# Optimization experiments

Hardware: AMD Instinct MI355X
Metric: run time of the kernel (lower is better)

The kernel has to match this reference:

```python
import jax, jax.numpy as jnp
import numpy as np

B, D, H = 256, 512, 256
K = 5
MARGIN = 1.0
TAU = 1.0
LAM_C = 0.01
LAM_E = 0.1
BETA = 0.1
LN_EPS = 1e-5


def _layernorm(x, g, b):
    mu = jnp.mean(x, axis=-1, keepdims=True)
    var = jnp.var(x, axis=-1, keepdims=True)
    return (x - mu) * jax.lax.rsqrt(var + LN_EPS) * g + b


def setup_inputs() -> dict:
    key = jax.random.key(0)
    ks = jax.random.split(key, 16)
    s = 0.02
    inp = {
        "outputs": jax.random.normal(ks[0], (B, 3, 64, 64), jnp.float32),
        "images": jax.random.normal(ks[1], (B, 3, 64, 64), jnp.float32),
        "f_orig": jax.random.normal(ks[2], (B, D), jnp.float32),
        "f_recon": jax.random.normal(ks[3], (B, D), jnp.float32),
        "cf1": jax.random.normal(ks[4], (B, 256, 8, 8), jnp.float32),
        "cf2": jax.random.normal(ks[5], (B, 512, 4, 4), jnp.float32),
        # EnergyNet encoder params
        "W1": jax.random.normal(ks[6], (D, H), jnp.float32) * s,
        "b1": jnp.zeros((H,), jnp.float32),
        "g1": jnp.ones((H,), jnp.float32),
        "be1": jnp.zeros((H,), jnp.float32),
        "W2": jax.random.normal(ks[7], (H, H), jnp.float32) * s,
        "b2": jnp.zeros((H,), jnp.float32),
        # EnergyNet interaction params
        "W3": jax.random.normal(ks[8], (3 * H, H), jnp.float32) * s,
        "b3": jnp.zeros((H,), jnp.float32),
        "g3": jnp.ones((H,), jnp.float32),
        "be3": jnp.zeros((H,), jnp.float32),
        "W4": jax.random.normal(ks[9], (H, H // 2), jnp.float32) * s,
        "b4": jnp.zeros((H // 2,), jnp.float32),
        "W5": jax.random.normal(ks[10], (H // 2, 1), jnp.float32) * s,
        "b5": jnp.zeros((1,), jnp.float32),
    }
    return inp


def _encoder(x, W1, b1, g1, be1, W2, b2):
    h = _layernorm(x @ W1 + b1, g1, be1)
    return jax.nn.relu(h) @ W2 + b2


def _energy_matrix(f1, f2, W1, b1, g1, be1, W2, b2, W3, b3, g3, be3, W4, b4, W5, b5):
    e1 = _encoder(f1, W1, b1, g1, be1, W2, b2)  # [B,H]
    e2 = _encoder(f2, W1, b1, g1, be1, W2, b2)  # [B,H]
    e1b = jnp.broadcast_to(e1[:, None, :], (B, B, H))
    e2b = jnp.broadcast_to(e2[None, :, :], (B, B, H))
    combined = jnp.concatenate([e1b, e2b, e1b * e2b], axis=-1)  # [B,B,3H]
    h = jax.nn.relu(_layernorm(combined @ W3 + b3, g3, be3))
    h = jax.nn.relu(h @ W4 + b4)
    return (h @ W5 + b5)[..., 0]  # [B,B]


def _topk_neighbors(f, k):
    fn = f / (jnp.linalg.norm(f, axis=1, keepdims=True))
    sim = fn @ fn.T
    sim = jnp.where(jnp.eye(f.shape[0], dtype=bool), -jnp.inf, sim)
    _, idx = jax.lax.top_k(sim, k)  # [B,k]
    onehot = jnp.zeros((f.shape[0], f.shape[0]), jnp.float32)
    rows = jnp.arange(f.shape[0])[:, None]
    return onehot.at[rows, idx].set(1.0)


def _entropy(x):
    xn = (x - x.min()) / (x.max() - x.min() + 1e-8)
    # torch.histc(bins=256, min=0, max=1): values at max go to last bin
    idx = jnp.clip(jnp.floor(xn.reshape(-1) * 256.0).astype(jnp.int32), 0, 255)
    hist = jnp.bincount(idx, length=256).astype(jnp.float32)
    p = hist / hist.sum()
    return -jnp.sum(p * jnp.log2(p + 1e-8))


def reference(outputs, images, f_orig, f_recon, cf1, cf2,
              W1, b1, g1, be1, W2, b2, W3, b3, g3, be3, W4, b4, W5, b5):
    # reconstruction loss
    recon = jnp.mean((outputs - images) ** 2)

    # energy margin loss
    E = _energy_matrix(f_orig, f_recon, W1, b1, g1, be1, W2, b2,
                       W3, b3, g3, be3, W4, b4, W5, b5)
    pos = jnp.diag(E)[:, None]
    losses = jax.nn.relu(MARGIN + E - pos)
    neg_mask = ~jnp.eye(B, dtype=bool)
    standard_loss = jnp.sum(losses * neg_mask) / (B * (B - 1))

    k = min(K, B - 1)
    on = _topk_neighbors(f_orig, k)
    rn = _topk_neighbors(f_recon, k)
    inter = jnp.sum(on * rn, axis=1)
    union = jnp.sum(jnp.clip(on + rn, 0.0, 1.0), axis=1)
    jaccard = inter / (union + 1e-8)
    neighbor_loss = 1.0 - jnp.mean(jaccard)
    energy_loss = standard_loss + 0.3 * neighbor_loss

    # compression loss over the dict of compressed features {cf1, cf2}
    sp = 0.5 * (jnp.mean(jnp.abs(cf1)) + jnp.mean(jnp.abs(cf2)))
    en = 0.5 * (_entropy(cf1) + _entropy(cf2))
    compress = sp + BETA * en

    total = recon + LAM_C * compress + LAM_E * energy_loss
    return (total, recon, energy_loss, compress)
```

## Files before the change

kernel.cpp:

```cpp
#include <hip/hip_runtime.h>
#include <math.h>

typedef __attribute__((ext_vector_type(8))) short short8;
typedef __attribute__((ext_vector_type(4))) float f32x4;


__device__ __forceinline__ float wave_sum(float v) {
#pragma unroll
    for (int o = 32; o > 0; o >>= 1) v += __shfl_down(v, o);
    return v;
}

__device__ __forceinline__ float block_sum256(float v, float* red) {
    v = wave_sum(v);
    int t = threadIdx.x;
    if ((t & 63) == 0) red[t >> 6] = v;
    __syncthreads();
    float r = red[0] + red[1] + red[2] + red[3];
    __syncthreads();
    return r;
}

__device__ __forceinline__ unsigned fenc(float f) {
    unsigned u = __float_as_uint(f);
    return (u & 0x80000000u) ? ~u : (u | 0x80000000u);
}
__device__ __forceinline__ float fdec(unsigned u) {
    return (u & 0x80000000u) ? __uint_as_float(u & 0x7fffffffu) : __uint_as_float(~u);
}

__device__ __forceinline__ ushort f2bf(float f) {
    unsigned u = __float_as_uint(f);
    unsigned r = (u + 0x7fffu + ((u >> 16) & 1u)) >> 16;
    return (ushort)r;
}


__global__ void init_kernel(float* wsf, unsigned* wsu, int* wsi) {
    int t = threadIdx.x;
    if (t < 7) wsf[t] = 0.f;
    if (t == 7 || t == 9) wsu[t] = 0xFFFFFFFFu;
    if (t == 8 || t == 10) wsu[t] = 0u;
    wsi[16 + t] = 0;
    wsi[272 + t] = 0;
}

__global__ void recon_kernel(const float4* __restrict__ o, const float4* __restrict__ im,
                             int n4, float* acc) {
    __shared__ float red[4];
    float s = 0.f;
    for (int i = blockIdx.x * blockDim.x + threadIdx.x; i < n4; i += gridDim.x * blockDim.x) {
        float4 a = o[i], b = im[i];
        float dx = a.x - b.x, dy = a.y - b.y, dz = a.z - b.z, dw = a.w - b.w;
        s += dx * dx + dy * dy + dz * dz + dw * dw;
    }
    float tot = block_sum256(s, red);
    if (threadIdx.x == 0) atomicAdd(acc, tot);
}

__global__ void absmm_kernel(const float4* __restrict__ x, int n4,
                             float* absAcc, unsigned* mnAcc, unsigned* mxAcc) {
    __shared__ float red[4];
    __shared__ float rmn[4], rmx[4];
    float s = 0.f, mn = INFINITY, mx = -INFINITY;
    for (int i = blockIdx.x * blockDim.x + threadIdx.x; i < n4; i += gridDim.x * blockDim.x) {
        float4 a = x[i];
        s += fabsf(a.x) + fabsf(a.y) + fabsf(a.z) + fabsf(a.w);
        mn = fminf(mn, fminf(fminf(a.x, a.y), fminf(a.z, a.w)));
        mx = fmaxf(mx, fmaxf(fmaxf(a.x, a.y), fmaxf(a.z, a.w)));
    }
    float tot = block_sum256(s, red);
#pragma unroll
    for (int o = 32; o > 0; o >>= 1) {
        mn = fminf(mn, __shfl_down(mn, o));
        mx = fmaxf(mx, __shfl_down(mx, o));
    }
    int t = threadIdx.x;
    if ((t & 63) == 0) { rmn[t >> 6] = mn; rmx[t >> 6] = mx; }
    __syncthreads();
    if (t == 0) {
        atomicAdd(absAcc, tot);
        float m1 = fminf(fminf(rmn[0], rmn[1]), fminf(rmn[2], rmn[3]));
        float m2 = fmaxf(fmaxf(rmx[0], rmx[1]), fmaxf(rmx[2], rmx[3]));
        atomicMin(mnAcc, fenc(m1));
        atomicMax(mxAcc, fenc(m2));
    }
}

__global__ void hist_kernel(const float4* __restrict__ x, int n4,
                            const unsigned* mm, int* hist) {
    __shared__ int hl[256];
    hl[threadIdx.x] = 0;
    __syncthreads();
    float mn = fdec(mm[0]), mx = fdec(mm[1]);
    float inv = 256.f / (mx - mn + 1e-8f);
    for (int i = blockIdx.x * blockDim.x + threadIdx.x; i < n4; i += gridDim.x * blockDim.x) {
        float4 a = x[i];
        int b0 = min(max((int)floorf((a.x - mn) * inv), 0), 255);
        int b1 = min(max((int)floorf((a.y - mn) * inv), 0), 255);
        int b2 = min(max((int)floorf((a.z - mn) * inv), 0), 255);
        int b3 = min(max((int)floorf((a.w - mn) * inv), 0), 255);
        atomicAdd(&hl[b0], 1);
        atomicAdd(&hl[b1], 1);
        atomicAdd(&hl[b2], 1);
        atomicAdd(&hl[b3], 1);
    }
    __syncthreads();
    if (hl[threadIdx.x]) atomicAdd(&hist[threadIdx.x], hl[threadIdx.x]);
}

__global__ void entropy_kernel(const int* h1, const int* h2, float* out, float n1, float n2) {
    __shared__ float red[4];
    int t = threadIdx.x;
    float p1 = (float)h1[t] / n1;
    float p2 = (float)h2[t] / n2;
    float e1 = -p1 * log2f(p1 + 1e-8f);
    float e2 = -p2 * log2f(p2 + 1e-8f);
    float s1 = block_sum256(e1, red);
    float s2 = block_sum256(e2, red);
    if (t == 0) { out[0] = s1; out[1] = s2; }
}

__global__ void norm_kernel(const float4* __restrict__ fo, const float4* __restrict__ fr,
                            float* rnorm) {
    __shared__ float red[4];
    int r = blockIdx.x;
    const float4* f = (r < 256) ? (fo + (size_t)r * 128) : (fr + (size_t)(r - 256) * 128);
    float s = 0.f;
    if (threadIdx.x < 128) {
        float4 a = f[threadIdx.x];
        s = a.x * a.x + a.y * a.y + a.z * a.z + a.w * a.w;
    }
    float tot = block_sum256(s, red);
    if (threadIdx.x == 0) rnorm[r] = 1.0f / sqrtf(tot);
}

__global__ void encoder_kernel(const float* __restrict__ f_orig, const float* __restrict__ f_recon,
                               const float* __restrict__ W1, const float* __restrict__ b1,
                               const float* __restrict__ g1, const float* __restrict__ be1,
                               const float* __restrict__ W2, const float* __restrict__ b2,
                               const float* __restrict__ W3,
                               float* __restrict__ eAll, float* __restrict__ Aall) {
    int r = blockIdx.x;
    int t = threadIdx.x;
    const float* f = (r < 256) ? (f_orig + (size_t)r * 512) : (f_recon + (size_t)(r - 256) * 512);
    const float* W3p = (r < 256) ? W3 : (W3 + 256 * 256);
    __shared__ float fs[512];
    __shared__ float hs[256];
    __shared__ float es[256];
    __shared__ float red[4];
    fs[t] = f[t];
    fs[t + 256] = f[t + 256];
    __syncthreads();
    float x = b1[t];
    for (int k = 0; k < 512; ++k) x += fs[k] * W1[k * 256 + t];
    float s1 = block_sum256(x, red);
    float s2 = block_sum256(x * x, red);
    float mean = s1 * (1.f / 256.f);
    float var = s2 * (1.f / 256.f) - mean * mean;
    float rstd = rsqrtf(var + 1e-5f);
    float hn = (x - mean) * rstd * g1[t] + be1[t];
    hs[t] = fmaxf(hn, 0.f);
    __syncthreads();
    float e = b2[t];
    for (int k = 0; k < 256; ++k) e += hs[k] * W2[k * 256 + t];
    eAll[(size_t)r * 256 + t] = e;
    es[t] = e;
    __syncthreads();
    float a = 0.f;
    for (int k = 0; k < 256; ++k) a += es[k] * W3p[k * 256 + t];
    Aall[(size_t)r * 256 + t] = a;
}

__global__ void topk_kernel(const float4* __restrict__ fo, const float4* __restrict__ fr,
                            const float* __restrict__ rnorm, float* jacAcc) {
    int i = blockIdx.x, t = threadIdx.x;
    __shared__ float4 fis[128];
    __shared__ float sv[256];
    __shared__ int si[256];
    __shared__ int O[5], R[5];
    for (int pass = 0; pass < 2; ++pass) {
        const float4* f = pass ? fr : fo;
        const float* rn = pass ? (rnorm + 256) : rnorm;
        if (t < 128) fis[t] = f[(size_t)i * 128 + t];
        __syncthreads();
        float dot = 0.f;
        const float4* frow = f + (size_t)t * 128;
        for (int k = 0; k < 128; ++k) {
            float4 a = fis[k], b = frow[k];
            dot += a.x * b.x + a.y * b.y + a.z * b.z + a.w * b.w;
        }
        float simv = dot * rn[i] * rn[t];
        if (t == i) simv = -INFINITY;
        int chosen = 0;
        for (int r5 = 0; r5 < 5; ++r5) {
            sv[t] = chosen ? -INFINITY : simv;
            si[t] = t;
            __syncthreads();
            for (int s = 128; s > 0; s >>= 1) {
                if (t < s) {
                    if (sv[t + s] > sv[t] || (sv[t + s] == sv[t] && si[t + s] < si[t])) {
                        sv[t] = sv[t + s];
                        si[t] = si[t + s];
                    }
                }
                __syncthreads();
            }
            int wIdx = si[0];
            if (t == wIdx) chosen = 1;
            if (t == 0) { if (pass) R[r5] = wIdx; else O[r5] = wIdx; }
            __syncthreads();
        }
        __syncthreads();
    }
    if (t == 0) {
        int inter = 0;
#pragma unroll
        for (int a = 0; a < 5; ++a)
#pragma unroll
            for (int b = 0; b < 5; ++b) inter += (O[a] == R[b]);
        float fi2 = (float)inter;
        float jac = fi2 / (10.f - fi2 + 1e-8f);
        atomicAdd(jacAcc, jac);
    }
}

__global__ void pack_w3_kernel(const float* __restrict__ W3c, ushort* __restrict__ W3p) {
    int s = blockIdx.x * 256 + threadIdx.x;
    int lane = s & 63;
    int tt = (s >> 6) & 15;
    int kk = s >> 10;
    int qq = lane >> 4, nn = lane & 15;
    int tcol = tt * 16 + nn;
    short8 v;
#pragma unroll
    for (int jj = 0; jj < 8; ++jj) {
        int k = kk * 32 + qq * 8 + jj;
        v[jj] = (short)f2bf(W3c[(size_t)k * 256 + tcol]);
    }
    *(short8*)(W3p + (size_t)s * 8) = v;
}

__global__ void pack_w4_kernel(const float* __restrict__ W4, ushort* __restrict__ W4p) {
    int s = blockIdx.x * 256 + threadIdx.x;
    int lane = s & 63;
    int tt = (s >> 6) & 7;
    int kk = s >> 9;
    int qq = lane >> 4, nn = lane & 15;
    int ncol = tt * 16 + nn;
    short8 v;
#pragma unroll
    for (int jj = 0; jj < 8; ++jj) {
        int k = kk * 32 + qq * 8 + jj;
        v[jj] = (short)f2bf(W4[(size_t)k * 128 + ncol]);
    }
    *(short8*)(W4p + (size_t)s * 8) = v;
}

__global__ __launch_bounds__(256) void energy_mfma_kernel(
    const float* __restrict__ eAll, const float* __restrict__ Aall,
    const ushort* __restrict__ W3p, const ushort* __restrict__ W4p,
    const float* __restrict__ b3, const float* __restrict__ g3, const float* __restrict__ be3,
    const float* __restrict__ b4, const float* __restrict__ W5, const float* __restrict__ b5,
    float* __restrict__ E)
{
    int i = blockIdx.x >> 2;
    int jq = blockIdx.x & 3;
    int t = threadIdx.x;
    int w = t >> 6;
    int lane = t & 63;
    int q = lane >> 4;
    int n = lane & 15;
    int jbase = jq * 64 + w * 16;

    __shared__ float comb[256], g3s[256], be3s[256];
    __shared__ uint4 Bst[1024];
    __shared__ __align__(16) ushort Hs[4][16 * 264];

    const float* e1 = eAll + (size_t)i * 256;
    const float* e2 = eAll + 65536;
    const float* A1 = Aall + (size_t)i * 256;
    const float* A2 = Aall + 65536;

    comb[t] = A1[t] + b3[t];
    g3s[t] = g3[t];
    be3s[t] = be3[t];

    f32x4 acc[16];
#pragma unroll
    for (int x = 0; x < 16; ++x) acc[x] = (f32x4){0.f, 0.f, 0.f, 0.f};

    const float* e2row = e2 + (size_t)(jbase + n) * 256;

    for (int kk = 0; kk < 8; ++kk) {
        __syncthreads();
        {
            const uint4* src = (const uint4*)(W3p + (size_t)kk * 8192);
#pragma unroll
            for (int x = 0; x < 4; ++x) Bst[t * 4 + x] = src[t * 4 + x];
        }
        int kb = kk * 32 + q * 8;
        float4 ea0 = *(const float4*)(e2row + kb);
        float4 ea1 = *(const float4*)(e2row + kb + 4);
        float4 eb0 = *(const float4*)(e1 + kb);
        float4 eb1 = *(const float4*)(e1 + kb + 4);
        short8 af;
        af[0] = (short)f2bf(ea0.x * eb0.x);
        af[1] = (short)f2bf(ea0.y * eb0.y);
        af[2] = (short)f2bf(ea0.z * eb0.z);
        af[3] = (short)f2bf(ea0.w * eb0.w);
        af[4] = (short)f2bf(ea1.x * eb1.x);
        af[5] = (short)f2bf(ea1.y * eb1.y);
        af[6] = (short)f2bf(ea1.z * eb1.z);
        af[7] = (short)f2bf(ea1.w * eb1.w);
        __syncthreads();
        const short8* bst = (const short8*)Bst;
#pragma unroll
        for (int tt = 0; tt < 16; ++tt) {
            short8 bfr = bst[tt * 64 + lane];
            acc[tt] = __builtin_amdgcn_mfma_f32_16x16x32_bf16(af, bfr, acc[tt], 0, 0, 0);
        }
    }

    float s1[4] = {0.f, 0.f, 0.f, 0.f}, s2[4] = {0.f, 0.f, 0.f, 0.f};
#pragma unroll
    for (int tt = 0; tt < 16; ++tt) {
        int col = tt * 16 + n;
        float cb = comb[col];
#pragma unroll
        for (int r = 0; r < 4; ++r) {
            int jr = jbase + q * 4 + r;
            float v = acc[tt][r] + cb + A2[(size_t)jr * 256 + col];
            acc[tt][r] = v;
            s1[r] += v;
            s2[r] += v * v;
        }
    }
#pragma unroll
    for (int off = 1; off < 16; off <<= 1) {
#pragma unroll
        for (int r = 0; r < 4; ++r) {
            s1[r] += __shfl_xor(s1[r], off);
            s2[r] += __shfl_xor(s2[r], off);
        }
    }
    float mean[4], rstd[4];
#pragma unroll
    for (int r = 0; r < 4; ++r) {
        mean[r] = s1[r] * (1.f / 256.f);
        float var = s2[r] * (1.f / 256.f) - mean[r] * mean[r];
        rstd[r] = rsqrtf(var + 1e-5f);
    }
    ushort* hrow = Hs[w];
#pragma unroll
    for (int tt = 0; tt < 16; ++tt) {
        int col = tt * 16 + n;
        float gg = g3s[col], be = be3s[col];
#pragma unroll
        for (int r = 0; r < 4; ++r) {
            float hv = fmaxf((acc[tt][r] - mean[r]) * rstd[r] * gg + be, 0.f);
            hrow[(q * 4 + r) * 264 + col] = f2bf(hv);
        }
    }

    f32x4 gacc[8];
#pragma unroll
    for (int x = 0; x < 8; ++x) gacc[x] = (f32x4){0.f, 0.f, 0.f, 0.f};

    for (int kk = 0; kk < 8; ++kk) {
        __syncthreads();
        {
            const uint4* src = (const uint4*)(W4p + (size_t)kk * 4096);
#pragma unroll
            for (int x = 0; x < 2; ++x) Bst[t * 2 + x] = src[t * 2 + x];
        }
        short8 af = *(const short8*)(hrow + n * 264 + kk * 32 + q * 8);
        __syncthreads();
        const short8* bst = (const short8*)Bst;
#pragma unroll
        for (int tt = 0; tt < 8; ++tt) {
            short8 bfr = bst[tt * 64 + lane];
            gacc[tt] = __builtin_amdgcn_mfma_f32_16x16x32_bf16(af, bfr, gacc[tt], 0, 0, 0);
        }
    }

    float ep[4] = {0.f, 0.f, 0.f, 0.f};
    float b5v = b5[0];
#pragma unroll
    for (int tt = 0; tt < 8; ++tt) {
        int col = tt * 16 + n;
        float b4v = b4[col], w5v = W5[col];
#pragma unroll
        for (int r = 0; r < 4; ++r)
            ep[r] += fmaxf(gacc[tt][r] + b4v, 0.f) * w5v;
    }
#pragma unroll
    for (int off = 1; off < 16; off <<= 1) {
#pragma unroll
        for (int r = 0; r < 4; ++r) ep[r] += __shfl_xor(ep[r], off);
    }
    if (n == 0) {
#pragma unroll
        for (int r = 0; r < 4; ++r)
            E[(size_t)i * 256 + jbase + q * 4 + r] = ep[r] + b5v;
    }
}

__global__ void margin_kernel(const float* __restrict__ E, float* slAcc) {
    __shared__ float red[4];
    int i = blockIdx.x, t = threadIdx.x;
    float diag = E[(size_t)i * 256 + i];
    float l = (t == i) ? 0.f : fmaxf(1.f + E[(size_t)i * 256 + t] - diag, 0.f);
    float tot = block_sum256(l, red);
    if (t == 0) atomicAdd(slAcc, tot);
}

__global__ void finalize_kernel(const float* wsf, float* out) {
    if (threadIdx.x == 0 && blockIdx.x == 0) {
        float recon = wsf[0] / 3145728.f;
        float sp = 0.5f * (wsf[1] / 4194304.f + wsf[2] / 2097152.f);
        float en = 0.5f * (wsf[3] + wsf[4]);
        float compress = sp + 0.1f * en;
        float sl = wsf[5] / (256.f * 255.f);
        float nl = 1.f - wsf[6] / 256.f;
        float energy = sl + 0.3f * nl;
        float total = recon + 0.01f * compress + 0.1f * energy;
        out[0] = total;
        out[1] = recon;
        out[2] = energy;
        out[3] = compress;
    }
}

extern "C" void kernel_launch(void* const* d_in, const int* in_sizes, int n_in,
                              void* d_out, int out_size, void* d_ws, size_t ws_size,
                              hipStream_t stream) {
    const float* outputs = (const float*)d_in[0];
    const float* images  = (const float*)d_in[1];
    const float* f_orig  = (const float*)d_in[2];
    const float* f_recon = (const float*)d_in[3];
    const float* cf1 = (const float*)d_in[4];
    const float* cf2 = (const float*)d_in[5];
    const float* W1 = (const float*)d_in[6];
    const float* b1 = (const float*)d_in[7];
    const float* g1 = (const float*)d_in[8];
    const float* be1 = (const float*)d_in[9];
    const float* W2 = (const float*)d_in[10];
    const float* b2 = (const float*)d_in[11];
    const float* W3 = (const float*)d_in[12];
    const float* b3 = (const float*)d_in[13];
    const float* g3 = (const float*)d_in[14];
    const float* be3 = (const float*)d_in[15];
    const float* W4 = (const float*)d_in[16];
    const float* b4 = (const float*)d_in[17];
    const float* W5 = (const float*)d_in[18];
    const float* b5 = (const float*)d_in[19];

    float* wsf = (float*)d_ws;
    unsigned* wsu = (unsigned*)d_ws;
    int* wsi = (int*)d_ws;
    float* out = (float*)d_out;

    float* rnorm = wsf + 528;
    float* eAll = wsf + 1040;
    float* Aall = wsf + 132112;
    float* Emat = wsf + 263184;
    ushort* W3pk = (ushort*)(wsf + 328720);
    ushort* W4pk = (ushort*)(wsf + 361488);

    hipLaunchKernelGGL(init_kernel, dim3(1), dim3(256), 0, stream, wsf, wsu, wsi);
    hipLaunchKernelGGL(pack_w3_kernel, dim3(32), dim3(256), 0, stream, W3 + 512 * 256, W3pk);
    hipLaunchKernelGGL(pack_w4_kernel, dim3(16), dim3(256), 0, stream, W4, W4pk);
    hipLaunchKernelGGL(recon_kernel, dim3(512), dim3(256), 0, stream,
                       (const float4*)outputs, (const float4*)images, 786432, wsf + 0);
    hipLaunchKernelGGL(absmm_kernel, dim3(512), dim3(256), 0, stream,
                       (const float4*)cf1, 1048576, wsf + 1, wsu + 7, wsu + 8);
    hipLaunchKernelGGL(absmm_kernel, dim3(512), dim3(256), 0, stream,
                       (const float4*)cf2, 524288, wsf + 2, wsu + 9, wsu + 10);
    hipLaunchKernelGGL(hist_kernel, dim3(512), dim3(256), 0, stream,
                       (const float4*)cf1, 1048576, wsu + 7, wsi + 16);
    hipLaunchKernelGGL(hist_kernel, dim3(512), dim3(256), 0, stream,
                       (const float4*)cf2, 524288, wsu + 9, wsi + 272);
    hipLaunchKernelGGL(entropy_kernel, dim3(1), dim3(256), 0, stream,
                       wsi + 16, wsi + 272, wsf + 3, 4194304.f, 2097152.f);
    hipLaunchKernelGGL(norm_kernel, dim3(512), dim3(256), 0, stream,
                       (const float4*)f_orig, (const float4*)f_recon, rnorm);
    hipLaunchKernelGGL(encoder_kernel, dim3(512), dim3(256), 0, stream,
                       f_orig, f_recon, W1, b1, g1, be1, W2, b2, W3, eAll, Aall);
    hipLaunchKernelGGL(topk_kernel, dim3(256), dim3(256), 0, stream,
                       (const float4*)f_orig, (const float4*)f_recon, rnorm, wsf + 6);
    hipLaunchKernelGGL(energy_mfma_kernel, dim3(1024), dim3(256), 0, stream,
                       eAll, Aall, W3pk, W4pk, b3, g3, be3, b4, W5, b5, Emat);
    hipLaunchKernelGGL(margin_kernel, dim3(256), dim3(256), 0, stream, Emat, wsf + 5);
    hipLaunchKernelGGL(finalize_kernel, dim3(1), dim3(1), 0, stream, wsf, out);
}
```

Before: 323.6 us.

## Fuse reduction kernels and rewrite top-k with transposed normalized features

Merges the recon, abs/min/max and norm reductions into one multi-role stats kernel, merges the two histogram kernels, the two weight-pack kernels, and entropy into finalize, which cuts the launch count. The top-k neighbor search is restructured: normalized features are transposed into a workspace so each block computes coalesced similarity rows for two query rows. Top-5 selection now uses wave shuffle reductions instead of repeated shared-memory tree reductions with many barriers. A separate jaccard kernel then combines the stored indices. This adds an extra transpose pass and extra workspace traffic.

After: 278.2 us. 1.16x faster.

```diff
diff --git a/kernel.cpp b/kernel.cpp
--- a/kernel.cpp
+++ b/kernel.cpp
@@ -45,94 +45,209 @@
     wsi[272 + t] = 0;
 }
 
-__global__ void recon_kernel(const float4* __restrict__ o, const float4* __restrict__ im,
-                             int n4, float* acc) {
-    __shared__ float red[4];
-    float s = 0.f;
-    for (int i = blockIdx.x * blockDim.x + threadIdx.x; i < n4; i += gridDim.x * blockDim.x) {
-        float4 a = o[i], b = im[i];
-        float dx = a.x - b.x, dy = a.y - b.y, dz = a.z - b.z, dw = a.w - b.w;
-        s += dx * dx + dy * dy + dz * dz + dw * dw;
-    }
-    float tot = block_sum256(s, red);
-    if (threadIdx.x == 0) atomicAdd(acc, tot);
-}
-
-__global__ void absmm_kernel(const float4* __restrict__ x, int n4,
-                             float* absAcc, unsigned* mnAcc, unsigned* mxAcc) {
+__global__ __launch_bounds__(256) void stats_kernel(
+    const float4* __restrict__ o, const float4* __restrict__ im,
+    const float4* __restrict__ cf1, const float4* __restrict__ cf2,
+    const float4* __restrict__ fo, const float4* __restrict__ fr,
+    float* wsf, unsigned* wsu, float* rnorm) {
     __shared__ float red[4];
     __shared__ float rmn[4], rmx[4];
-    float s = 0.f, mn = INFINITY, mx = -INFINITY;
-    for (int i = blockIdx.x * blockDim.x + threadIdx.x; i < n4; i += gridDim.x * blockDim.x) {
+    int b = blockIdx.x, t = threadIdx.x;
+    if (b < 512) {
+        float s = 0.f;
+        for (int i = b * 256 + t; i < 786432; i += 512 * 256) {
+            float4 a = o[i], c = im[i];
+            float dx = a.x - c.x, dy = a.y - c.y, dz = a.z - c.z, dw = a.w - c.w;
+            s += dx * dx + dy * dy + dz * dz + dw * dw;
+        }
+        float tot = block_sum256(s, red);
+        if (t == 0) atomicAdd(wsf + 0, tot);
+    } else if (b < 1536) {
+        int which = (b < 1024) ? 0 : 1;
+        const float4* x = which ? cf2 : cf1;
+        int n4 = which ? 524288 : 1048576;
+        int b0 = which ? 1024 : 512;
+        float s = 0.f, mn = INFINITY, mx = -INFINITY;
+        for (int i = (b - b0) * 256 + t; i < n4; i += 512 * 256) {
+            float4 a = x[i];
+            s += fabsf(a.x) + fabsf(a.y) + fabsf(a.z) + fabsf(a.w);
+            mn = fminf(mn, fminf(fminf(a.x, a.y), fminf(a.z, a.w)));
+            mx = fmaxf(mx, fmaxf(fmaxf(a.x, a.y), fmaxf(a.z, a.w)));
+        }
+        float tot = block_sum256(s, red);
+#pragma unroll
+        for (int off = 32; off > 0; off >>= 1) {
+            mn = fminf(mn, __shfl_down(mn, off));
+            mx = fmaxf(mx, __shfl_down(mx, off));
+        }
+        if ((t & 63) == 0) { rmn[t >> 6] = mn; rmx[t >> 6] = mx; }
+        __syncthreads();
+        if (t == 0) {
+            atomicAdd(wsf + 1 + which, tot);
+            float m1 = fminf(fminf(rmn[0], rmn[1]), fminf(rmn[2], rmn[3]));
+            float m2 = fmaxf(fmaxf(rmx[0], rmx[1]), fmaxf(rmx[2], rmx[3]));
+            atomicMin(wsu + 7 + which * 2, fenc(m1));
+            atomicMax(wsu + 8 + which * 2, fenc(m2));
+        }
+    } else {
+        int r = b - 1536;
+        const float4* f = (r < 256) ? (fo + (size_t)r * 128) : (fr + (size_t)(r - 256) * 128);
+        float s = 0.f;
+        if (t < 128) {
+            float4 a = f[t];
+            s = a.x * a.x + a.y * a.y + a.z * a.z + a.w * a.w;
+        }
+        float tot = block_sum256(s, red);
+        if (t == 0) rnorm[r] = 1.0f / sqrtf(tot);
+    }
+}
+
+__global__ __launch_bounds__(256) void hist_kernel(const float4* __restrict__ cf1,
+                                                   const float4* __restrict__ cf2,
+                                                   const unsigned* wsu, int* wsi) {
+    __shared__ int hl[256];
+    int b = blockIdx.x, t = threadIdx.x;
+    hl[t] = 0;
+    __syncthreads();
+    int which = (b < 512) ? 0 : 1;
+    const float4* x = which ? cf2 : cf1;
+    int n4 = which ? 524288 : 1048576;
+    int b0 = which ? 512 : 0;
+    int* hist = wsi + (which ? 272 : 16);
+    float mn = fdec(wsu[7 + which * 2]), mx = fdec(wsu[8 + which * 2]);
+    float inv = 256.f / (mx - mn + 1e-8f);
+    for (int i = (b - b0) * 256 + t; i < n4; i += 512 * 256) {
         float4 a = x[i];
-        s += fabsf(a.x) + fabsf(a.y) + fabsf(a.z) + fabsf(a.w);
-        mn = fminf(mn, fminf(fminf(a.x, a.y), fminf(a.z, a.w)));
-        mx = fmaxf(mx, fmaxf(fmaxf(a.x, a.y), fmaxf(a.z, a.w)));
-    }
-    float tot = block_sum256(s, red);
-#pragma unroll
-    for (int o = 32; o > 0; o >>= 1) {
-        mn = fminf(mn, __shfl_down(mn, o));
-        mx = fmaxf(mx, __shfl_down(mx, o));
-    }
-    int t = threadIdx.x;
-    if ((t & 63) == 0) { rmn[t >> 6] = mn; rmx[t >> 6] = mx; }
-    __syncthreads();
-    if (t == 0) {
-        atomicAdd(absAcc, tot);
-        float m1 = fminf(fminf(rmn[0], rmn[1]), fminf(rmn[2], rmn[3]));
-        float m2 = fmaxf(fmaxf(rmx[0], rmx[1]), fmaxf(rmx[2], rmx[3]));
-        atomicMin(mnAcc, fenc(m1));
-        atomicMax(mxAcc, fenc(m2));
-    }
-}
-
-__global__ void hist_kernel(const float4* __restrict__ x, int n4,
-                            const unsigned* mm, int* hist) {
-    __shared__ int hl[256];
-    hl[threadIdx.x] = 0;
-    __syncthreads();
-    float mn = fdec(mm[0]), mx = fdec(mm[1]);
-    float inv = 256.f / (mx - mn + 1e-8f);
-    for (int i = blockIdx.x * blockDim.x + threadIdx.x; i < n4; i += gridDim.x * blockDim.x) {
-        float4 a = x[i];
-        int b0 = min(max((int)floorf((a.x - mn) * inv), 0), 255);
-        int b1 = min(max((int)floorf((a.y - mn) * inv), 0), 255);
-        int b2 = min(max((int)floorf((a.z - mn) * inv), 0), 255);
-        int b3 = min(max((int)floorf((a.w - mn) * inv), 0), 255);
-        atomicAdd(&hl[b0], 1);
-        atomicAdd(&hl[b1], 1);
-        atomicAdd(&hl[b2], 1);
-        atomicAdd(&hl[b3], 1);
-    }
-    __syncthreads();
-    if (hl[threadIdx.x]) atomicAdd(&hist[threadIdx.x], hl[threadIdx.x]);
-}
-
-__global__ void entropy_kernel(const int* h1, const int* h2, float* out, float n1, float n2) {
+        int b0i = min(max((int)floorf((a.x - mn) * inv), 0), 255);
+        int b1i = min(max((int)floorf((a.y - mn) * inv), 0), 255);
+        int b2i = min(max((int)floorf((a.z - mn) * inv), 0), 255);
+        int b3i = min(max((int)floorf((a.w - mn) * inv), 0), 255);
+        atomicAdd(&hl[b0i], 1);
+        atomicAdd(&hl[b1i], 1);
+        atomicAdd(&hl[b2i], 1);
+        atomicAdd(&hl[b3i], 1);
+    }
+    __syncthreads();
+    if (hl[t]) atomicAdd(&hist[t], hl[t]);
+}
+
+__global__ __launch_bounds__(256) void transpose_kernel(const float* __restrict__ fo,
+                                                        const float* __restrict__ fr,
+                                                        const float* __restrict__ rnorm,
+                                                        float* __restrict__ fnT) {
+    int b = blockIdx.x;
+    int pass = b >> 6;
+    int kt = (b >> 2) & 15;
+    int jt = b & 3;
+    int k0 = kt * 32, j0 = jt * 64;
+    const float* f = pass ? fr : fo;
+    const float* rn = rnorm + pass * 256;
+    __shared__ float tile[64][33];
+    int t = threadIdx.x;
+    int cl = t & 31, rl = t >> 5;
+#pragma unroll
+    for (int r = 0; r < 8; ++r) {
+        int row = j0 + rl + r * 8;
+        tile[rl + r * 8][cl] = f[(size_t)row * 512 + k0 + cl] * rn[row];
+    }
+    __syncthreads();
+    int jl = t & 63, kq = t >> 6;
+    float* dst = fnT + (size_t)pass * 131072;
+#pragma unroll
+    for (int c = 0; c < 8; ++c) {
+        int kl = kq * 8 + c;
+        dst[(size_t)(k0 + kl) * 256 + j0 + jl] = tile[jl][kl];
+    }
+}
+
+__global__ __launch_bounds__(256) void simtop_kernel(const float* __restrict__ fo,
+                                                     const float* __restrict__ fr,
+                                                     const float* __restrict__ rnorm,
+                                                     const float* __restrict__ fnT,
+                                                     int* __restrict__ top5) {
+    int b = blockIdx.x;
+    int pass = b >> 7, pair = b & 127;
+    int i0 = pair * 2, i1 = i0 + 1;
+    const float* f = pass ? fr : fo;
+    const float* rn = rnorm + pass * 256;
+    __shared__ float2 fs2[512];
+    __shared__ float candV[4][2][5];
+    __shared__ int candI[4][2][5];
+    int t = threadIdx.x;
+    float rn0 = rn[i0], rn1 = rn[i1];
+    const float* f0 = f + (size_t)i0 * 512;
+    const float* f1 = f + (size_t)i1 * 512;
+    fs2[t] = make_float2(f0[t] * rn0, f1[t] * rn1);
+    fs2[t + 256] = make_float2(f0[t + 256] * rn0, f1[t + 256] * rn1);
+    __syncthreads();
+    int j = t;
+    const float* col = fnT + (size_t)pass * 131072 + j;
+    float a0 = 0.f, a1 = 0.f;
+#pragma unroll 16
+    for (int k = 0; k < 512; ++k) {
+        float v = col[(size_t)k * 256];
+        float2 fv = fs2[k];
+        a0 += fv.x * v;
+        a1 += fv.y * v;
+    }
+    if (j == i0) a0 = -INFINITY;
+    if (j == i1) a1 = -INFINITY;
+    int w = t >> 6, lane = t & 63;
+    for (int sel = 0; sel < 2; ++sel) {
+        float v2 = sel ? a1 : a0;
+        int idx = j;
+        for (int r = 0; r < 5; ++r) {
+            float m = v2;
+            int mi = idx;
+#pragma unroll
+            for (int off = 32; off > 0; off >>= 1) {
+                float om = __shfl_xor(m, off);
+                int omi = __shfl_xor(mi, off);
+                if (om > m || (om == m && omi < mi)) { m = om; mi = omi; }
+            }
+            if (lane == 0) { candV[w][sel][r] = m; candI[w][sel][r] = mi; }
+            if (idx == mi) v2 = -INFINITY;
+        }
+    }
+    __syncthreads();
+    if (w < 2) {
+        float v = -INFINITY;
+        int ix = 0x7fffffff;
+        if (lane < 20) { v = candV[lane / 5][w][lane % 5]; ix = candI[lane / 5][w][lane % 5]; }
+        int iSel = w ? i1 : i0;
+        for (int r = 0; r < 5; ++r) {
+            float m = v;
+            int mi = ix;
+#pragma unroll
+            for (int off = 32; off > 0; off >>= 1) {
+                float om = __shfl_xor(m, off);
+                int omi = __shfl_xor(mi, off);
+                if (om > m || (om == m && omi < mi)) { m = om; mi = omi; }
+            }
+            if (lane == 0) top5[((size_t)pass * 256 + iSel) * 5 + r] = mi;
+            if (ix == mi) v = -INFINITY;
+        }
+    }
+}
+
+__global__ void jaccard_kernel(const int* __restrict__ top5, float* jacOut) {
     __shared__ float red[4];
-    int t = threadIdx.x;
-    float p1 = (float)h1[t] / n1;
-    float p2 = (float)h2[t] / n2;
-    float e1 = -p1 * log2f(p1 + 1e-8f);
-    float e2 = -p2 * log2f(p2 + 1e-8f);
-    float s1 = block_sum256(e1, red);
-    float s2 = block_sum256(e2, red);
-    if (t == 0) { out[0] = s1; out[1] = s2; }
-}
-
-__global__ void norm_kernel(const float4* __restrict__ fo, const float4* __restrict__ fr,
-                            float* rnorm) {
-    __shared__ float red[4];
-    int r = blockIdx.x;
-    const float4* f = (r < 256) ? (fo + (size_t)r * 128) : (fr + (size_t)(r - 256) * 128);
-    float s = 0.f;
-    if (threadIdx.x < 128) {
-        float4 a = f[threadIdx.x];
-        s = a.x * a.x + a.y * a.y + a.z * a.z + a.w * a.w;
-    }
-    float tot = block_sum256(s, red);
-    if (threadIdx.x == 0) rnorm[r] = 1.0f / sqrtf(tot);
+    int i = threadIdx.x;
+    int O[5], R[5];
+#pragma unroll
+    for (int r = 0; r < 5; ++r) {
+        O[r] = top5[i * 5 + r];
+        R[r] = top5[(256 + i) * 5 + r];
+    }
+    int inter = 0;
+#pragma unroll
+    for (int a = 0; a < 5; ++a)
+#pragma unroll
+        for (int bq = 0; bq < 5; ++bq) inter += (O[a] == R[bq]);
+    float fi2 = (float)inter;
+    float jac = fi2 / (10.f - fi2 + 1e-8f);
+    float s = block_sum256(jac, red);
+    if (i == 0) jacOut[0] = s;
 }
 
 __global__ void encoder_kernel(const float* __restrict__ f_orig, const float* __restrict__ f_recon,
@@ -172,89 +287,38 @@
     Aall[(size_t)r * 256 + t] = a;
 }
 
-__global__ void topk_kernel(const float4* __restrict__ fo, const float4* __restrict__ fr,
-                            const float* __restrict__ rnorm, float* jacAcc) {
-    int i = blockIdx.x, t = threadIdx.x;
-    __shared__ float4 fis[128];
-    __shared__ float sv[256];
-    __shared__ int si[256];
-    __shared__ int O[5], R[5];
-    for (int pass = 0; pass < 2; ++pass) {
-        const float4* f = pass ? fr : fo;
-        const float* rn = pass ? (rnorm + 256) : rnorm;
-        if (t < 128) fis[t] = f[(size_t)i * 128 + t];
-        __syncthreads();
-        float dot = 0.f;
-        const float4* frow = f + (size_t)t * 128;
-        for (int k = 0; k < 128; ++k) {
-            float4 a = fis[k], b = frow[k];
-            dot += a.x * b.x + a.y * b.y + a.z * b.z + a.w * b.w;
-        }
-        float simv = dot * rn[i] * rn[t];
-        if (t == i) simv = -INFINITY;
-        int chosen = 0;
-        for (int r5 = 0; r5 < 5; ++r5) {
-            sv[t] = chosen ? -INFINITY : simv;
-            si[t] = t;
-            __syncthreads();
-            for (int s = 128; s > 0; s >>= 1) {
-                if (t < s) {
-                    if (sv[t + s] > sv[t] || (sv[t + s] == sv[t] && si[t + s] < si[t])) {
-                        sv[t] = sv[t + s];
-                        si[t] = si[t + s];
-                    }
-                }
-                __syncthreads();
-            }
-            int wIdx = si[0];
-            if (t == wIdx) chosen = 1;
-            if (t == 0) { if (pass) R[r5] = wIdx; else O[r5] = wIdx; }
-            __syncthreads();
-        }
-        __syncthreads();
-    }
-    if (t == 0) {
-        int inter = 0;
-#pragma unroll
-        for (int a = 0; a < 5; ++a)
-#pragma unroll
-            for (int b = 0; b < 5; ++b) inter += (O[a] == R[b]);
-        float fi2 = (float)inter;
-        float jac = fi2 / (10.f - fi2 + 1e-8f);
-        atomicAdd(jacAcc, jac);
-    }
-}
-
-__global__ void pack_w3_kernel(const float* __restrict__ W3c, ushort* __restrict__ W3p) {
-    int s = blockIdx.x * 256 + threadIdx.x;
-    int lane = s & 63;
-    int tt = (s >> 6) & 15;
-    int kk = s >> 10;
-    int qq = lane >> 4, nn = lane & 15;
-    int tcol = tt * 16 + nn;
-    short8 v;
-#pragma unroll
-    for (int jj = 0; jj < 8; ++jj) {
-        int k = kk * 32 + qq * 8 + jj;
-        v[jj] = (short)f2bf(W3c[(size_t)k * 256 + tcol]);
-    }
-    *(short8*)(W3p + (size_t)s * 8) = v;
-}
-
-__global__ void pack_w4_kernel(const float* __restrict__ W4, ushort* __restrict__ W4p) {
-    int s = blockIdx.x * 256 + threadIdx.x;
-    int lane = s & 63;
-    int tt = (s >> 6) & 7;
-    int kk = s >> 9;
-    int qq = lane >> 4, nn = lane & 15;
-    int ncol = tt * 16 + nn;
-    short8 v;
-#pragma unroll
-    for (int jj = 0; jj < 8; ++jj) {
-        int k = kk * 32 + qq * 8 + jj;
-        v[jj] = (short)f2bf(W4[(size_t)k * 128 + ncol]);
-    }
-    *(short8*)(W4p + (size_t)s * 8) = v;
+__global__ void pack_kernel(const float* __restrict__ W3c, const float* __restrict__ W4,
+                            ushort* __restrict__ W3p, ushort* __restrict__ W4p) {
+    int b = blockIdx.x, t = threadIdx.x;
+    if (b < 32) {
+        int s = b * 256 + t;
+        int lane = s & 63;
+        int tt = (s >> 6) & 15;
+        int kk = s >> 10;
+        int qq = lane >> 4, nn = lane & 15;
+        int tcol = tt * 16 + nn;
+        short8 v;
+#pragma unroll
+        for (int jj = 0; jj < 8; ++jj) {
+            int k = kk * 32 + qq * 8 + jj;
+            v[jj] = (short)f2bf(W3c[(size_t)k * 256 + tcol]);
+        }
+        *(short8*)(W3p + (size_t)s * 8) = v;
+    } else {
+        int s = (b - 32) * 256 + t;
+        int lane = s & 63;
+        int tt = (s >> 6) & 7;
+        int kk = s >> 9;
+        int qq = lane >> 4, nn = lane & 15;
+        int ncol = tt * 16 + nn;
+        short8 v;
+#pragma unroll
+        for (int jj = 0; jj < 8; ++jj) {
+            int k = kk * 32 + qq * 8 + jj;
+            v[jj] = (short)f2bf(W4[(size_t)k * 128 + ncol]);
+        }
+        *(short8*)(W4p + (size_t)s * 8) = v;
+    }
 }
 
 __global__ __launch_bounds__(256) void energy_mfma_kernel(
@@ -415,11 +479,17 @@
     if (t == 0) atomicAdd(slAcc, tot);
 }
 
-__global__ void finalize_kernel(const float* wsf, float* out) {
-    if (threadIdx.x == 0 && blockIdx.x == 0) {
+__global__ void finalize_kernel(const float* wsf, const int* h1, const int* h2, float* out) {
+    __shared__ float red[4];
+    int t = threadIdx.x;
+    float p1 = (float)h1[t] / 4194304.f;
+    float p2 = (float)h2[t] / 2097152.f;
+    float s1 = block_sum256(-p1 * log2f(p1 + 1e-8f), red);
+    float s2 = block_sum256(-p2 * log2f(p2 + 1e-8f), red);
+    if (t == 0) {
         float recon = wsf[0] / 3145728.f;
         float sp = 0.5f * (wsf[1] / 4194304.f + wsf[2] / 2097152.f);
-        float en = 0.5f * (wsf[3] + wsf[4]);
+        float en = 0.5f * (s1 + s2);
         float compress = sp + 0.1f * en;
         float sl = wsf[5] / (256.f * 255.f);
         float nl = 1.f - wsf[6] / 256.f;
@@ -467,30 +537,29 @@
     float* Emat = wsf + 263184;
     ushort* W3pk = (ushort*)(wsf + 328720);
     ushort* W4pk = (ushort*)(wsf + 361488);
+    float* fnT = wsf + 377872;
+    int* top5 = wsi + 640016;
 
     hipLaunchKernelGGL(init_kernel, dim3(1), dim3(256), 0, stream, wsf, wsu, wsi);
-    hipLaunchKernelGGL(pack_w3_kernel, dim3(32), dim3(256), 0, stream, W3 + 512 * 256, W3pk);
-    hipLaunchKernelGGL(pack_w4_kernel, dim3(16), dim3(256), 0, stream, W4, W4pk);
-    hipLaunchKernelGGL(recon_kernel, dim3(512), dim3(256), 0, stream,
-                       (const float4*)outputs, (const float4*)images, 786432, wsf + 0);
-    hipLaunchKernelGGL(absmm_kernel, dim3(512), dim3(256), 0, stream,
-                       (const float4*)cf1, 1048576, wsf + 1, wsu + 7, wsu + 8);
-    hipLaunchKernelGGL(absmm_kernel, dim3(512), dim3(256), 0, stream,
-                       (const float4*)cf2, 524288, wsf + 2, wsu + 9, wsu + 10);
-    hipLaunchKernelGGL(hist_kernel, dim3(512), dim3(256), 0, stream,
-                       (const float4*)cf1, 1048576, wsu + 7, wsi + 16);
-    hipLaunchKernelGGL(hist_kernel, dim3(512), dim3(256), 0, stream,
-                       (const float4*)cf2, 524288, wsu + 9, wsi + 272);
-    hipLaunchKernelGGL(entropy_kernel, dim3(1), dim3(256), 0, stream,
-                       wsi + 16, wsi + 272, wsf + 3, 4194304.f, 2097152.f);
-    hipLaunchKernelGGL(norm_kernel, dim3(512), dim3(256), 0, stream,
-                       (const float4*)f_orig, (const float4*)f_recon, rnorm);
+    hipLaunchKernelGGL(pack_kernel, dim3(48), dim3(256), 0, stream,
+                       W3 + 512 * 256, W4, W3pk, W4pk);
+    hipLaunchKernelGGL(stats_kernel, dim3(2048), dim3(256), 0, stream,
+                       (const float4*)outputs, (const float4*)images,
+                       (const float4*)cf1, (const float4*)cf2,
+                       (const float4*)f_orig, (const float4*)f_recon,
+                       wsf, wsu, rnorm);
+    hipLaunchKernelGGL(hist_kernel, dim3(1024), dim3(256), 0, stream,
+                       (const float4*)cf1, (const float4*)cf2, wsu, wsi);
+    hipLaunchKernelGGL(transpose_kernel, dim3(128), dim3(256), 0, stream,
+                       f_orig, f_recon, rnorm, fnT);
     hipLaunchKernelGGL(encoder_kernel, dim3(512), dim3(256), 0, stream,
                        f_orig, f_recon, W1, b1, g1, be1, W2, b2, W3, eAll, Aall);
-    hipLaunchKernelGGL(topk_kernel, dim3(256), dim3(256), 0, stream,
-                       (const float4*)f_orig, (const float4*)f_recon, rnorm, wsf + 6);
+    hipLaunchKernelGGL(simtop_kernel, dim3(256), dim3(256), 0, stream,
+                       f_orig, f_recon, rnorm, fnT, top5);
     hipLaunchKernelGGL(energy_mfma_kernel, dim3(1024), dim3(256), 0, stream,
                        eAll, Aall, W3pk, W4pk, b3, g3, be3, b4, W5, b5, Emat);
     hipLaunchKernelGGL(margin_kernel, dim3(256), dim3(256), 0, stream, Emat, wsf + 5);
-    hipLaunchKernelGGL(finalize_kernel, dim3(1), dim3(1), 0, stream, wsf, out);
-}
+    hipLaunchKernelGGL(jaccard_kernel, dim3(1), dim3(256), 0, stream, top5, wsf + 6);
+    hipLaunchKernelGGL(finalize_kernel, dim3(1), dim3(256), 0, stream,
+                       wsf, wsi + 16, wsi + 272, out);
+}
```
